# Kernel tuning notes

Measured on AMD Instinct MI355X. Metric: run time of the kernel, lower is better.

## Reference

```python
import jax, jax.numpy as jnp
import numpy as np

N_NODES = 100000
N_EDGES = 1600000
D_IN = 32
D_OUT = 32
K_HOPS = 2
CUTGRAPH = 0.2
EPS = 1e-12  # torch F.normalize eps


def setup_inputs() -> dict:
    key = jax.random.key(0)
    k1, k2, k3, k4 = jax.random.split(key, 4)
    features = jax.random.normal(k1, (N_NODES, D_IN), dtype=jnp.float32)
    W = jax.random.normal(k2, (D_OUT, D_IN), dtype=jnp.float32) * (1.0 / np.sqrt(D_IN))
    src = jax.random.randint(k3, (N_EDGES,), 0, N_NODES, dtype=jnp.int64 if jax.config.jax_enable_x64 else jnp.int32)
    dst = jax.random.randint(k4, (N_EDGES,), 0, N_NODES, dtype=jnp.int64 if jax.config.jax_enable_x64 else jnp.int32)
    return {"features": features, "W": W, "src": src, "dst": dst}


def reference(features, W, src, dst):
    N = features.shape[0]
    E = src.shape[0]
    cut_k = int(E * CUTGRAPH)  # static edge count to prune

    # symmetric degree norm: deg^{-1/2} over in-degrees, clamped at 1
    deg = jax.ops.segment_sum(jnp.ones((E,), features.dtype), dst, num_segments=N)
    norm = jnp.power(jnp.clip(deg, 1.0, None), -0.5)[:, None]  # [N,1]

    h = features
    for _ in range(K_HOPS):
        # cosine-similarity edge pruning: zero the cut_k lowest-cos edges
        nrm = jnp.linalg.norm(h, axis=-1, keepdims=True)
        nh = h / jnp.maximum(nrm, EPS)  # F.normalize(p=2)
        cos = jnp.sum(nh[src] * nh[dst], axis=-1)  # [E]
        _, low_idx = jax.lax.top_k(-cos, cut_k)    # indices of smallest cos
        w = jnp.ones((E,), h.dtype).at[low_idx].set(0.0)

        h = h * norm
        msg = h[src] * w[:, None]                       # u_mul_e gather [E,D]
        h = jax.ops.segment_sum(msg, dst, num_segments=N)  # sum scatter
        h = h * norm

    return h @ W.T  # fc (bias=False)
```

## Files before the change

kernel.cpp:

```cpp
#include <hip/hip_runtime.h>
#include <hip/hip_bf16.h>
#include <stdint.h>

#define N_NODES 100000
#define N_EDGES 1600000
#define D_FEAT 32
#define CUT_K 320000
#define COSKEY_NB 3125
#define HC_NB 1000
#define HC_SLICE 1600
#define SCAN_NB ((N_NODES + 255) / 256)
#define TAILCAP 400000

struct SelState { unsigned long long prefix; unsigned int k; };

__global__ void deg_kernel(const int* __restrict__ dst, int* __restrict__ deg,
                           int* __restrict__ rank, int E) {
    int e = blockIdx.x * blockDim.x + threadIdx.x;
    if (e < E) rank[e] = atomicAdd(&deg[dst[e]], 1);
}

__global__ void blocksum_kernel(const int* __restrict__ deg, int* __restrict__ bsum,
                                float* __restrict__ nrm, int N) {
    int i = blockIdx.x * 256 + threadIdx.x;
    int v = (i < N) ? deg[i] : 0;
    if (i < N) nrm[i] = 1.0f / sqrtf(fmaxf((float)v, 1.0f));
#pragma unroll
    for (int off = 32; off > 0; off >>= 1) v += __shfl_down(v, off, 64);
    __shared__ int ws4[4];
    if ((threadIdx.x & 63) == 0) ws4[threadIdx.x >> 6] = v;
    __syncthreads();
    if (threadIdx.x == 0) bsum[blockIdx.x] = ws4[0] + ws4[1] + ws4[2] + ws4[3];
}

__global__ void writeoffs_kernel(const int* __restrict__ deg, const int* __restrict__ bsum,
                                 int* __restrict__ offs, int N) {
    __shared__ int buf[256];
    __shared__ int ws4[4];
    __shared__ int sboff;
    int t = threadIdx.x;
    int b = blockIdx.x;
    int partial = 0;
    for (int i = t; i < b; i += 256) partial += bsum[i];
#pragma unroll
    for (int off = 32; off > 0; off >>= 1) partial += __shfl_down(partial, off, 64);
    if ((t & 63) == 0) ws4[t >> 6] = partial;
    __syncthreads();
    if (t == 0) sboff = ws4[0] + ws4[1] + ws4[2] + ws4[3];
    __syncthreads();
    int i = b * 256 + t;
    int v = (i < N) ? deg[i] : 0;
    buf[t] = v;
    __syncthreads();
    for (int off = 1; off < 256; off <<= 1) {
        int u = (t >= off) ? buf[t - off] : 0;
        __syncthreads();
        buf[t] += u;
        __syncthreads();
    }
    int ex = buf[t] - v + sboff;
    if (i < N) offs[i] = ex;
    if (i == N - 1) offs[N] = ex + v;
}

__global__ void fill_kernel(const int* __restrict__ src, const int* __restrict__ dst,
                            const int* __restrict__ rank, const int* __restrict__ offs,
                            uint4* __restrict__ csr, int E) {
    int e = blockIdx.x * blockDim.x + threadIdx.x;
    if (e >= E) return;
    int d = dst[e];
    int pos = offs[d] + rank[e];
    csr[pos] = make_uint4((unsigned int)src[e], (unsigned int)d, (unsigned int)e, 0u);
}

__global__ void rownorm_kernel(const float* __restrict__ h, float* __restrict__ nh, int N) {
    int i = blockIdx.x * blockDim.x + threadIdx.x;
    if (i >= N) return;
    const float4* hp = (const float4*)(h + (size_t)i * D_FEAT);
    float4 v[8];
    float ss = 0.f;
#pragma unroll
    for (int q = 0; q < 8; ++q) {
        v[q] = hp[q];
        ss += v[q].x * v[q].x + v[q].y * v[q].y + v[q].z * v[q].z + v[q].w * v[q].w;
    }
    float inv = 1.0f / fmaxf(sqrtf(ss), 1e-12f);
    float4* op = (float4*)(nh + (size_t)i * D_FEAT);
#pragma unroll
    for (int q = 0; q < 8; ++q) {
        float4 ov = v[q];
        ov.x *= inv; ov.y *= inv; ov.z *= inv; ov.w *= inv;
        op[q] = ov;
    }
}

__device__ __forceinline__ unsigned long long scan_select(
        const unsigned int* __restrict__ hist,
        unsigned long long pfx_in, unsigned int k_in,
        unsigned int* k_out) {
    __shared__ unsigned int sbuf[256];
    __shared__ unsigned long long s_pfx;
    __shared__ unsigned int s_k;
    int t = threadIdx.x;
    unsigned int s = hist[t];
    sbuf[t] = s;
    __syncthreads();
    for (int off = 1; off < 256; off <<= 1) {
        unsigned int v = (t >= off) ? sbuf[t - off] : 0u;
        __syncthreads();
        sbuf[t] += v;
        __syncthreads();
    }
    unsigned int incl = sbuf[t];
    unsigned int excl = incl - s;
    if (excl < k_in && k_in <= incl) {
        s_pfx = (pfx_in << 8) | (unsigned long long)t;
        s_k = k_in - excl;
    }
    __syncthreads();
    if (k_out) *k_out = s_k;
    return s_pfx;
}

__global__ void coskey_kernel(const float* __restrict__ nh, const uint4* __restrict__ csr,
                              unsigned long long* __restrict__ keys,
                              unsigned int* __restrict__ hist0, int E) {
    __shared__ unsigned int lh[4][256];
    int t = threadIdx.x;
#pragma unroll
    for (int w = 0; w < 4; ++w) lh[w][t] = 0u;
    __syncthreads();
    int wave = t >> 6;
    int p0 = (blockIdx.x * 256 + t) * 2;
    uint4 r0 = csr[p0];
    uint4 r1 = csr[p0 + 1];
    const float4* a0 = (const float4*)(nh + (size_t)r0.x * D_FEAT);
    const float4* b0 = (const float4*)(nh + (size_t)r0.y * D_FEAT);
    const float4* a1 = (const float4*)(nh + (size_t)r1.x * D_FEAT);
    const float4* b1 = (const float4*)(nh + (size_t)r1.y * D_FEAT);
    float s0 = 0.f, s1 = 0.f;
#pragma unroll
    for (int q = 0; q < 8; ++q) {
        float4 x0 = a0[q], y0 = b0[q];
        s0 += x0.x * y0.x + x0.y * y0.y + x0.z * y0.z + x0.w * y0.w;
        float4 x1 = a1[q], y1 = b1[q];
        s1 += x1.x * y1.x + x1.y * y1.y + x1.z * y1.z + x1.w * y1.w;
    }
    unsigned int u0 = __float_as_uint(s0);
    unsigned int so0 = (u0 & 0x80000000u) ? ~u0 : (u0 | 0x80000000u);
    unsigned long long k0 = ((unsigned long long)so0 << 32) | r0.z;
    unsigned int u1 = __float_as_uint(s1);
    unsigned int so1 = (u1 & 0x80000000u) ? ~u1 : (u1 | 0x80000000u);
    unsigned long long k1 = ((unsigned long long)so1 << 32) | r1.z;
    *(ulonglong2*)(keys + p0) = make_ulonglong2(k0, k1);
    atomicAdd(&lh[wave][(unsigned int)(k0 >> 56)], 1u);
    atomicAdd(&lh[wave][(unsigned int)(k1 >> 56)], 1u);
    __syncthreads();
    unsigned int tot = lh[0][t] + lh[1][t] + lh[2][t] + lh[3][t];
    if (tot) atomicAdd(&hist0[t], tot);
}

__global__ void histc_kernel(const unsigned long long* __restrict__ in,
                             const int* __restrict__ cnt_in,
                             unsigned long long* __restrict__ out,
                             int* __restrict__ cnt_out,
                             const SelState* __restrict__ st_in,
                             SelState* __restrict__ st_out,
                             const unsigned int* __restrict__ hist_prev,
                             unsigned int* __restrict__ hist_cur, int pass) {
    __shared__ unsigned int lh[4][256];
    __shared__ unsigned int lcnt;
    int t = threadIdx.x, b = blockIdx.x;
#pragma unroll
    for (int w = 0; w < 4; ++w) lh[w][t] = 0u;
    if (t == 0) lcnt = 0u;

    unsigned long long pfx_in = st_in ? st_in->prefix : 0ull;
    unsigned int k_in = st_in ? st_in->k : (unsigned int)CUT_K;
    unsigned int k_cur;
    unsigned long long prefix = scan_select(hist_prev, pfx_in, k_in, &k_cur);
    if (b == 0 && t == 0) { st_out->prefix = prefix; st_out->k = k_cur; }
    __syncthreads();

    int n = cnt_in ? cnt_in[b] : HC_SLICE;
    const unsigned long long* sin = in + (size_t)b * HC_SLICE;
    unsigned long long* sout = out + (size_t)b * HC_SLICE;
    int wave = t >> 6;
    int fshift = 64 - 8 * pass;
    int dshift = 56 - 8 * pass;
    for (int i = t; i < n; i += 256) {
        unsigned long long key = sin[i];
        if ((key >> fshift) == prefix) {
            atomicAdd(&lh[wave][(unsigned int)((key >> dshift) & 0xFFull)], 1u);
            unsigned int slot = atomicAdd(&lcnt, 1u);
            sout[slot] = key;
        }
    }
    __syncthreads();
    if (t == 0) cnt_out[b] = (int)lcnt;
    unsigned int tot = lh[0][t] + lh[1][t] + lh[2][t] + lh[3][t];
    if (tot) atomicAdd(&hist_cur[t], tot);
}

__global__ void tail_kernel(const unsigned long long* __restrict__ in_sl,
                            const int* __restrict__ cnt_in,
                            unsigned long long* __restrict__ dense,
                            const SelState* __restrict__ st2,
                            const unsigned int* __restrict__ hist2,
                            unsigned long long* __restrict__ kth_out) {
    __shared__ unsigned int lh[256];
    __shared__ unsigned int sbuf[256];
    __shared__ unsigned long long s_pfx;
    __shared__ unsigned int s_k;
    __shared__ unsigned int s_n;
    int t = threadIdx.x;

    unsigned long long pfx = st2->prefix;
    unsigned int k = st2->k;
    {
        unsigned int s = hist2[t];
        sbuf[t] = s;
        __syncthreads();
        for (int off = 1; off < 256; off <<= 1) {
            unsigned int v = (t >= off) ? sbuf[t - off] : 0u;
            __syncthreads();
            sbuf[t] += v;
            __syncthreads();
        }
        unsigned int incl = sbuf[t], excl = incl - s;
        if (excl < k && k <= incl) { s_pfx = (pfx << 8) | (unsigned long long)t; s_k = k - excl; }
        __syncthreads();
        pfx = s_pfx; k = s_k;
        __syncthreads();
    }

    unsigned int n_in = 0;
    for (int pass = 3; pass < 8; ++pass) {
        lh[t] = 0u;
        if (t == 0) s_n = 0u;
        __syncthreads();
        int fshift = 64 - 8 * pass;
        int dshift = 56 - 8 * pass;
        unsigned long long* outp = dense + ((pass & 1) ? 0 : TAILCAP);
        if (pass == 3) {
            for (int b = t; b < HC_NB; b += 256) {
                int n = cnt_in[b];
                const unsigned long long* sl = in_sl + (size_t)b * HC_SLICE;
                for (int i = 0; i < n; ++i) {
                    unsigned long long key = sl[i];
                    if ((key >> fshift) == pfx) {
                        atomicAdd(&lh[(unsigned int)((key >> dshift) & 0xFFull)], 1u);
                        unsigned int slot = atomicAdd(&s_n, 1u);
                        if (slot < TAILCAP) outp[slot] = key;
                    }
                }
            }
        } else {
            const unsigned long long* inp = dense + ((pass & 1) ? TAILCAP : 0);
            for (unsigned int i = t; i < n_in; i += 256) {
                unsigned long long key = inp[i];
                if ((key >> fshift) == pfx) {
                    atomicAdd(&lh[(unsigned int)((key >> dshift) & 0xFFull)], 1u);
                    unsigned int slot = atomicAdd(&s_n, 1u);
                    if (slot < TAILCAP) outp[slot] = key;
                }
            }
        }
        __syncthreads();
        n_in = s_n;
        unsigned int s = lh[t];
        sbuf[t] = s;
        __syncthreads();
        for (int off = 1; off < 256; off <<= 1) {
            unsigned int v = (t >= off) ? sbuf[t - off] : 0u;
            __syncthreads();
            sbuf[t] += v;
            __syncthreads();
        }
        unsigned int incl = sbuf[t], excl = incl - s;
        if (excl < k && k <= incl) { s_pfx = (pfx << 8) | (unsigned long long)t; s_k = k - excl; }
        __syncthreads();
        pfx = s_pfx; k = s_k;
        __syncthreads();
    }
    if (t == 0) *kth_out = pfx;
}

template<bool FUSE_FC>
__global__ void aggregate_csr_kernel(const float* __restrict__ h_in, float* __restrict__ h_out,
                                     const int* __restrict__ offs,
                                     const uint4* __restrict__ csr,
                                     const unsigned long long* __restrict__ keys,
                                     const unsigned long long* __restrict__ kth_in,
                                     const float* __restrict__ nrm,
                                     const float* __restrict__ W, int N) {
    __shared__ float Ws[32][33];
    __shared__ float hrow[8][33];
    int t = threadIdx.x;
    if (FUSE_FC) {
        for (int i = t; i < 1024; i += 256) Ws[i >> 5][i & 31] = W[i];
        __syncthreads();
    }
    unsigned long long kth = *kth_in;
    int g = blockIdx.x * 8 + (t >> 5);
    int j = t & 31;
    if (!FUSE_FC && g >= N) return;
    int lo = offs[g], hi = offs[g + 1];
    float acc = 0.f;
    int p = lo;
    for (; p + 8 <= hi; p += 8) {
        unsigned long long kk[8];
        unsigned int ss[8];
#pragma unroll
        for (int u = 0; u < 8; ++u) { kk[u] = keys[p + u]; ss[u] = csr[p + u].x; }
        float vv[8];
#pragma unroll
        for (int u = 0; u < 8; ++u) vv[u] = h_in[(size_t)ss[u] * D_FEAT + j] * nrm[ss[u]];
#pragma unroll
        for (int u = 0; u < 8; ++u) acc += (kk[u] > kth) ? vv[u] : 0.f;
    }
    for (; p < hi; ++p) {
        if (keys[p] > kth) {
            unsigned int s = csr[p].x;
            acc += h_in[(size_t)s * D_FEAT + j] * nrm[s];
        }
    }
    float val = acc * nrm[g];
    if (!FUSE_FC) {
        h_out[(size_t)g * D_FEAT + j] = val;
        return;
    }
    hrow[t >> 5][j] = val;
    __syncthreads();
    float oacc = 0.f;
#pragma unroll
    for (int q = 0; q < 32; ++q) oacc += hrow[t >> 5][q] * Ws[j][q];
    h_out[(size_t)g * D_FEAT + j] = oacc;
}

extern "C" void kernel_launch(void* const* d_in, const int* in_sizes, int n_in,
                              void* d_out, int out_size, void* d_ws, size_t ws_size,
                              hipStream_t stream) {
    const float* features = (const float*)d_in[0];
    const float* W        = (const float*)d_in[1];
    const int*   src      = (const int*)d_in[2];
    const int*   dst      = (const int*)d_in[3];
    float*       out      = (float*)d_out;

    char* ws = (char*)d_ws;
    size_t o = 0;
    auto take = [&](size_t bytes) -> char* {
        char* p = ws + o;
        o += (bytes + 255) & ~(size_t)255;
        return p;
    };
    int*                deg     = (int*)take((size_t)N_NODES * 4);
    float*              nrm     = (float*)take((size_t)N_NODES * 4);
    int*                offs    = (int*)take((size_t)(N_NODES + 1) * 4);
    int*                rank    = (int*)take((size_t)N_EDGES * 4);
    uint4*              csr     = (uint4*)take((size_t)N_EDGES * 16);
    float*              hA      = (float*)take((size_t)N_NODES * D_FEAT * 4);
    float*              hB      = (float*)take((size_t)N_NODES * D_FEAT * 4);
    float*              nh      = (float*)take((size_t)N_NODES * D_FEAT * 4);
    unsigned long long* keys    = (unsigned long long*)take((size_t)N_EDGES * 8);
    unsigned int*       hist    = (unsigned int*)take((size_t)16 * 256 * 4);
    SelState*           stArr   = (SelState*)take((size_t)16 * sizeof(SelState));
    unsigned long long* kthbuf  = (unsigned long long*)take(256);
    int*                bsum    = (int*)take((size_t)SCAN_NB * 4);
    int*                cnt_a   = (int*)take((size_t)HC_NB * 4);
    int*                cnt_b   = (int*)take((size_t)HC_NB * 4);

    unsigned long long* candA = (unsigned long long*)nh;
    unsigned long long* candB = (unsigned long long*)hB;

    hipMemsetAsync(deg, 0, (size_t)N_NODES * 4, stream);
    hipMemsetAsync(hist, 0, (size_t)16 * 256 * 4, stream);

    deg_kernel<<<(N_EDGES + 255) / 256, 256, 0, stream>>>(dst, deg, rank, N_EDGES);
    blocksum_kernel<<<SCAN_NB, 256, 0, stream>>>(deg, bsum, nrm, N_NODES);
    writeoffs_kernel<<<SCAN_NB, 256, 0, stream>>>(deg, bsum, offs, N_NODES);
    fill_kernel<<<(N_EDGES + 255) / 256, 256, 0, stream>>>(src, dst, rank, offs, csr, N_EDGES);

    const float* hin = features;
    for (int hop = 0; hop < 2; ++hop) {
        unsigned int* hh = hist + (size_t)hop * 8 * 256;
        SelState*     hst = stArr + (size_t)hop * 8;
        rownorm_kernel<<<(N_NODES + 255) / 256, 256, 0, stream>>>(hin, nh, N_NODES);
        coskey_kernel<<<COSKEY_NB, 256, 0, stream>>>(nh, csr, keys, hh, N_EDGES);
        histc_kernel<<<HC_NB, 256, 0, stream>>>(keys, nullptr, candA, cnt_a,
                                                nullptr, hst + 1,
                                                hh + 0 * 256, hh + 1 * 256, 1);
        histc_kernel<<<HC_NB, 256, 0, stream>>>(candA, cnt_a, candB, cnt_b,
                                                hst + 1, hst + 2,
                                                hh + 1 * 256, hh + 2 * 256, 2);
        tail_kernel<<<1, 256, 0, stream>>>(candB, cnt_b, candA,
                                           hst + 2, hh + 2 * 256, kthbuf + hop);
        if (hop == 0) {
            aggregate_csr_kernel<false><<<(N_NODES + 7) / 8, 256, 0, stream>>>(
                hin, hA, offs, csr, keys, kthbuf + hop, nrm, nullptr, N_NODES);
            hin = hA;
        } else {
            aggregate_csr_kernel<true><<<(N_NODES + 7) / 8, 256, 0, stream>>>(
                hin, out, offs, csr, keys, kthbuf + hop, nrm, W, N_NODES);
        }
    }
}
```

Before: 508.1 us.

## Pack CSR records into 64-bit and fuse row normalization into cosine kernel

Packs each CSR entry (src, dst, edge id) into a single 64-bit word instead of a 16-byte uint4, halving CSR traffic in the cosine and aggregation kernels. Removes the separate row-normalization kernel and the normalized-feature buffer; the cosine kernel now computes both endpoint norms on the fly from raw features. In exchange, each edge reads its two feature rows twice and does redundant per-edge norm computations, relying on cache for the second pass. Candidate buffers get dedicated workspace instead of aliasing the freed arrays.

```diff
diff --git a/kernel.cpp b/kernel.cpp
--- a/kernel.cpp
+++ b/kernel.cpp
@@ -12,6 +12,12 @@
 #define SCAN_NB ((N_NODES + 255) / 256)
 #define TAILCAP 400000
 
+#define PK(s, d, e) ((((unsigned long long)(s)) << 38) | \
+                     (((unsigned long long)(d)) << 21) | (unsigned long long)(e))
+#define PK_SRC(p) ((unsigned int)((p) >> 38))
+#define PK_DST(p) ((unsigned int)(((p) >> 21) & 0x1FFFFu))
+#define PK_EID(p) ((unsigned int)((p) & 0x1FFFFFu))
+
 struct SelState { unsigned long long prefix; unsigned int k; };
 
 __global__ void deg_kernel(const int* __restrict__ dst, int* __restrict__ deg,
@@ -65,33 +71,12 @@
 
 __global__ void fill_kernel(const int* __restrict__ src, const int* __restrict__ dst,
                             const int* __restrict__ rank, const int* __restrict__ offs,
-                            uint4* __restrict__ csr, int E) {
+                            unsigned long long* __restrict__ csr8, int E) {
     int e = blockIdx.x * blockDim.x + threadIdx.x;
     if (e >= E) return;
     int d = dst[e];
     int pos = offs[d] + rank[e];
-    csr[pos] = make_uint4((unsigned int)src[e], (unsigned int)d, (unsigned int)e, 0u);
-}
-
-__global__ void rownorm_kernel(const float* __restrict__ h, float* __restrict__ nh, int N) {
-    int i = blockIdx.x * blockDim.x + threadIdx.x;
-    if (i >= N) return;
-    const float4* hp = (const float4*)(h + (size_t)i * D_FEAT);
-    float4 v[8];
-    float ss = 0.f;
-#pragma unroll
-    for (int q = 0; q < 8; ++q) {
-        v[q] = hp[q];
-        ss += v[q].x * v[q].x + v[q].y * v[q].y + v[q].z * v[q].z + v[q].w * v[q].w;
-    }
-    float inv = 1.0f / fmaxf(sqrtf(ss), 1e-12f);
-    float4* op = (float4*)(nh + (size_t)i * D_FEAT);
-#pragma unroll
-    for (int q = 0; q < 8; ++q) {
-        float4 ov = v[q];
-        ov.x *= inv; ov.y *= inv; ov.z *= inv; ov.w *= inv;
-        op[q] = ov;
-    }
+    csr8[pos] = PK((unsigned int)src[e], (unsigned int)d, (unsigned int)e);
 }
 
 __device__ __forceinline__ unsigned long long scan_select(
@@ -122,7 +107,8 @@
     return s_pfx;
 }
 
-__global__ void coskey_kernel(const float* __restrict__ nh, const uint4* __restrict__ csr,
+__global__ void coskey_kernel(const float* __restrict__ h,
+                              const unsigned long long* __restrict__ csr8,
                               unsigned long long* __restrict__ keys,
                               unsigned int* __restrict__ hist0, int E) {
     __shared__ unsigned int lh[4][256];
@@ -132,26 +118,44 @@
     __syncthreads();
     int wave = t >> 6;
     int p0 = (blockIdx.x * 256 + t) * 2;
-    uint4 r0 = csr[p0];
-    uint4 r1 = csr[p0 + 1];
-    const float4* a0 = (const float4*)(nh + (size_t)r0.x * D_FEAT);
-    const float4* b0 = (const float4*)(nh + (size_t)r0.y * D_FEAT);
-    const float4* a1 = (const float4*)(nh + (size_t)r1.x * D_FEAT);
-    const float4* b1 = (const float4*)(nh + (size_t)r1.y * D_FEAT);
+    unsigned long long r0 = csr8[p0];
+    unsigned long long r1 = csr8[p0 + 1];
+    const float4* a0 = (const float4*)(h + (size_t)PK_SRC(r0) * D_FEAT);
+    const float4* b0 = (const float4*)(h + (size_t)PK_DST(r0) * D_FEAT);
+    const float4* a1 = (const float4*)(h + (size_t)PK_SRC(r1) * D_FEAT);
+    const float4* b1 = (const float4*)(h + (size_t)PK_DST(r1) * D_FEAT);
+    float sa0 = 0.f, sb0 = 0.f, sa1 = 0.f, sb1 = 0.f;
+#pragma unroll
+    for (int q = 0; q < 8; ++q) {
+        float4 x = a0[q]; sa0 += x.x * x.x + x.y * x.y + x.z * x.z + x.w * x.w;
+        float4 y = b0[q]; sb0 += y.x * y.x + y.y * y.y + y.z * y.z + y.w * y.w;
+        float4 z = a1[q]; sa1 += z.x * z.x + z.y * z.y + z.z * z.z + z.w * z.w;
+        float4 w4 = b1[q]; sb1 += w4.x * w4.x + w4.y * w4.y + w4.z * w4.z + w4.w * w4.w;
+    }
+    float ia0 = 1.0f / fmaxf(sqrtf(sa0), 1e-12f);
+    float ib0 = 1.0f / fmaxf(sqrtf(sb0), 1e-12f);
+    float ia1 = 1.0f / fmaxf(sqrtf(sa1), 1e-12f);
+    float ib1 = 1.0f / fmaxf(sqrtf(sb1), 1e-12f);
     float s0 = 0.f, s1 = 0.f;
 #pragma unroll
     for (int q = 0; q < 8; ++q) {
-        float4 x0 = a0[q], y0 = b0[q];
-        s0 += x0.x * y0.x + x0.y * y0.y + x0.z * y0.z + x0.w * y0.w;
-        float4 x1 = a1[q], y1 = b1[q];
-        s1 += x1.x * y1.x + x1.y * y1.y + x1.z * y1.z + x1.w * y1.w;
+        float4 xa = a0[q], xb = b0[q];
+        float4 na, nb;
+        na.x = xa.x * ia0; na.y = xa.y * ia0; na.z = xa.z * ia0; na.w = xa.w * ia0;
+        nb.x = xb.x * ib0; nb.y = xb.y * ib0; nb.z = xb.z * ib0; nb.w = xb.w * ib0;
+        s0 += na.x * nb.x + na.y * nb.y + na.z * nb.z + na.w * nb.w;
+        float4 ya = a1[q], yb = b1[q];
+        float4 ma, mb;
+        ma.x = ya.x * ia1; ma.y = ya.y * ia1; ma.z = ya.z * ia1; ma.w = ya.w * ia1;
+        mb.x = yb.x * ib1; mb.y = yb.y * ib1; mb.z = yb.z * ib1; mb.w = yb.w * ib1;
+        s1 += ma.x * mb.x + ma.y * mb.y + ma.z * mb.z + ma.w * mb.w;
     }
     unsigned int u0 = __float_as_uint(s0);
     unsigned int so0 = (u0 & 0x80000000u) ? ~u0 : (u0 | 0x80000000u);
-    unsigned long long k0 = ((unsigned long long)so0 << 32) | r0.z;
+    unsigned long long k0 = ((unsigned long long)so0 << 32) | PK_EID(r0);
     unsigned int u1 = __float_as_uint(s1);
     unsigned int so1 = (u1 & 0x80000000u) ? ~u1 : (u1 | 0x80000000u);
-    unsigned long long k1 = ((unsigned long long)so1 << 32) | r1.z;
+    unsigned long long k1 = ((unsigned long long)so1 << 32) | PK_EID(r1);
     *(ulonglong2*)(keys + p0) = make_ulonglong2(k0, k1);
     atomicAdd(&lh[wave][(unsigned int)(k0 >> 56)], 1u);
     atomicAdd(&lh[wave][(unsigned int)(k1 >> 56)], 1u);
@@ -289,7 +293,7 @@
 template<bool FUSE_FC>
 __global__ void aggregate_csr_kernel(const float* __restrict__ h_in, float* __restrict__ h_out,
                                      const int* __restrict__ offs,
-                                     const uint4* __restrict__ csr,
+                                     const unsigned long long* __restrict__ csr8,
                                      const unsigned long long* __restrict__ keys,
                                      const unsigned long long* __restrict__ kth_in,
                                      const float* __restrict__ nrm,
@@ -312,7 +316,7 @@
         unsigned long long kk[8];
         unsigned int ss[8];
 #pragma unroll
-        for (int u = 0; u < 8; ++u) { kk[u] = keys[p + u]; ss[u] = csr[p + u].x; }
+        for (int u = 0; u < 8; ++u) { kk[u] = keys[p + u]; ss[u] = PK_SRC(csr8[p + u]); }
         float vv[8];
 #pragma unroll
         for (int u = 0; u < 8; ++u) vv[u] = h_in[(size_t)ss[u] * D_FEAT + j] * nrm[ss[u]];
@@ -321,7 +325,7 @@
     }
     for (; p < hi; ++p) {
         if (keys[p] > kth) {
-            unsigned int s = csr[p].x;
+            unsigned int s = PK_SRC(csr8[p]);
             acc += h_in[(size_t)s * D_FEAT + j] * nrm[s];
         }
     }
@@ -358,11 +362,11 @@
     float*              nrm     = (float*)take((size_t)N_NODES * 4);
     int*                offs    = (int*)take((size_t)(N_NODES + 1) * 4);
     int*                rank    = (int*)take((size_t)N_EDGES * 4);
-    uint4*              csr     = (uint4*)take((size_t)N_EDGES * 16);
+    unsigned long long* csr8    = (unsigned long long*)take((size_t)N_EDGES * 8);
     float*              hA      = (float*)take((size_t)N_NODES * D_FEAT * 4);
-    float*              hB      = (float*)take((size_t)N_NODES * D_FEAT * 4);
-    float*              nh      = (float*)take((size_t)N_NODES * D_FEAT * 4);
     unsigned long long* keys    = (unsigned long long*)take((size_t)N_EDGES * 8);
+    unsigned long long* candA   = (unsigned long long*)take((size_t)HC_NB * HC_SLICE * 8);
+    unsigned long long* candB   = (unsigned long long*)take((size_t)HC_NB * HC_SLICE * 8);
     unsigned int*       hist    = (unsigned int*)take((size_t)16 * 256 * 4);
     SelState*           stArr   = (SelState*)take((size_t)16 * sizeof(SelState));
     unsigned long long* kthbuf  = (unsigned long long*)take(256);
@@ -370,23 +374,19 @@
     int*                cnt_a   = (int*)take((size_t)HC_NB * 4);
     int*                cnt_b   = (int*)take((size_t)HC_NB * 4);
 
-    unsigned long long* candA = (unsigned long long*)nh;
-    unsigned long long* candB = (unsigned long long*)hB;
-
     hipMemsetAsync(deg, 0, (size_t)N_NODES * 4, stream);
     hipMemsetAsync(hist, 0, (size_t)16 * 256 * 4, stream);
 
     deg_kernel<<<(N_EDGES + 255) / 256, 256, 0, stream>>>(dst, deg, rank, N_EDGES);
     blocksum_kernel<<<SCAN_NB, 256, 0, stream>>>(deg, bsum, nrm, N_NODES);
     writeoffs_kernel<<<SCAN_NB, 256, 0, stream>>>(deg, bsum, offs, N_NODES);
-    fill_kernel<<<(N_EDGES + 255) / 256, 256, 0, stream>>>(src, dst, rank, offs, csr, N_EDGES);
+    fill_kernel<<<(N_EDGES + 255) / 256, 256, 0, stream>>>(src, dst, rank, offs, csr8, N_EDGES);
 
     const float* hin = features;
     for (int hop = 0; hop < 2; ++hop) {
         unsigned int* hh = hist + (size_t)hop * 8 * 256;
         SelState*     hst = stArr + (size_t)hop * 8;
-        rownorm_kernel<<<(N_NODES + 255) / 256, 256, 0, stream>>>(hin, nh, N_NODES);
-        coskey_kernel<<<COSKEY_NB, 256, 0, stream>>>(nh, csr, keys, hh, N_EDGES);
+        coskey_kernel<<<COSKEY_NB, 256, 0, stream>>>(hin, csr8, keys, hh, N_EDGES);
         histc_kernel<<<HC_NB, 256, 0, stream>>>(keys, nullptr, candA, cnt_a,
                                                 nullptr, hst + 1,
                                                 hh + 0 * 256, hh + 1 * 256, 1);
@@ -397,11 +397,11 @@
                                            hst + 2, hh + 2 * 256, kthbuf + hop);
         if (hop == 0) {
             aggregate_csr_kernel<false><<<(N_NODES + 7) / 8, 256, 0, stream>>>(
-                hin, hA, offs, csr, keys, kthbuf + hop, nrm, nullptr, N_NODES);
+                hin, hA, offs, csr8, keys, kthbuf + hop, nrm, nullptr, N_NODES);
             hin = hA;
         } else {
             aggregate_csr_kernel<true><<<(N_NODES + 7) / 8, 256, 0, stream>>>(
-                hin, out, offs, csr, keys, kthbuf + hop, nrm, W, N_NODES);
-        }
-    }
-}
+                hin, out, offs, csr8, keys, kthbuf + hop, nrm, W, N_NODES);
+        }
+    }
+}
```

Result: slower. 535.7 us (+5.4%).
